# Optimization experiments

Hardware: AMD Instinct MI355X
Metric: run time of the kernel (lower is better)

Reference implementation:

```python
import jax, jax.numpy as jnp
import numpy as np

N = 50000      # nodes
E = 800000     # edges (before self loops)
D = 128        # node feat dim (in = hidden = out)
R_IN = 64      # edge feat in
R_OUT = 64     # edge feat out


def setup_inputs() -> dict:
    key = jax.random.key(0)
    ks = jax.random.split(key, 10)
    src = jax.random.randint(ks[0], (E,), 0, N, dtype=jnp.int32)
    dst = jax.random.randint(ks[1], (E,), 0, N, dtype=jnp.int32)
    x = jax.random.normal(ks[2], (N, D), jnp.float32)
    text_h = jax.random.normal(ks[3], (E, R_IN), jnp.float32)
    s = 1.0 / np.sqrt(D)
    W1 = jax.random.normal(ks[4], (D, D), jnp.float32) * s
    b1 = jnp.zeros((D,), jnp.float32)
    W2 = jax.random.normal(ks[5], (D, D), jnp.float32) * s
    b2 = jnp.zeros((D,), jnp.float32)
    sr = 1.0 / np.sqrt(R_IN)
    relW = jax.random.normal(ks[6], (R_IN, R_OUT), jnp.float32) * sr
    relb = jnp.zeros((R_OUT,), jnp.float32)
    return {"src": src, "dst": dst, "x": x, "text_h": text_h,
            "W1": W1, "b1": b1, "W2": W2, "b2": b2,
            "relW": relW, "relb": relb}


def _graph_conv(h, src, dst, norm_src, norm_dst, W, b, n):
    # DGL GraphConv, norm='both': scale src, gather, segment-sum to dst, scale dst, linear, relu
    h = h * norm_src                                   # [N, D]
    agg = jax.ops.segment_sum(h[src], dst, num_segments=n)  # [N, D]
    h = agg * norm_dst
    return jax.nn.relu(h @ W + b)


def reference(src, dst, x, text_h, W1, b1, W2, b2, relW, relb):
    n = x.shape[0]
    loop = jnp.arange(n, dtype=src.dtype)
    src_a = jnp.concatenate([src, loop])               # add_self_loop
    dst_a = jnp.concatenate([dst, loop])
    ones = jnp.ones(src_a.shape[0], x.dtype)
    out_deg = jax.ops.segment_sum(ones, src_a, num_segments=n)
    in_deg = jax.ops.segment_sum(ones, dst_a, num_segments=n)
    norm_src = (out_deg ** -0.5)[:, None]              # >=1 thanks to self loops
    norm_dst = (in_deg ** -0.5)[:, None]
    h = _graph_conv(x, src_a, dst_a, norm_src, norm_dst, W1, b1, n)
    h = _graph_conv(h, src_a, dst_a, norm_src, norm_dst, W2, b2, n)
    # apply_edges: rel_linear on text_h (self-loop edges get zero-filled text_h)
    text_all = jnp.concatenate([text_h, jnp.zeros((n, text_h.shape[1]), text_h.dtype)])
    e_h = text_all @ relW + relb                       # [E+N, R_OUT]
    # apply_nodes: activation applied once more
    h = jax.nn.relu(h)
    return h, e_h
```

## Files before the change

### kernel.cpp

```cpp
#include <hip/hip_runtime.h>

constexpr int D = 128;
constexpr int R = 64;
constexpr int CAP = 64;
constexpr int OVF_CAP = 65536;
constexpr int TPAD = 68;

typedef float floatx4 __attribute__((ext_vector_type(4)));

static __device__ __forceinline__ float4 f4fma(float a, float4 w, float4 c) {
  c.x = fmaf(a, w.x, c.x); c.y = fmaf(a, w.y, c.y);
  c.z = fmaf(a, w.z, c.z); c.w = fmaf(a, w.w, c.w);
  return c;
}

static __device__ __forceinline__ void nt_store4(float4 v, float* p) {
  floatx4 q; q.x = v.x; q.y = v.y; q.z = v.z; q.w = v.w;
  __builtin_nontemporal_store(q, (floatx4*)p);
}

__global__ void k_init(int* deg_out, int* cursor, int* ovf_cnt, int n) {
  int i = blockIdx.x * blockDim.x + threadIdx.x;
  if (i < n) { deg_out[i] = 1; cursor[i] = 0; }
  if (i == 0) ovf_cnt[0] = 0;
}

__global__ void k_fill(const int* __restrict__ src, const int* __restrict__ dst,
                       int* deg_out, int* cursor, int* bucket,
                       int* ovf_cnt, int2* ovf, int e) {
  int i = blockIdx.x * blockDim.x + threadIdx.x;
  if (i >= e) return;
  int d = dst[i], s = src[i];
  atomicAdd(&deg_out[s], 1);
  int slot = atomicAdd(&cursor[d], 1);
  if (slot < CAP) bucket[(size_t)d * CAP + slot] = s;
  else {
    int oi = atomicAdd(ovf_cnt, 1);
    if (oi < OVF_CAP) ovf[oi] = make_int2(s, d);
  }
}

__global__ void k_norm(const int* __restrict__ deg_out, const int* __restrict__ cursor,
                       float* ns, float* nd, int n) {
  int i = blockIdx.x * blockDim.x + threadIdx.x;
  if (i < n) {
    ns[i] = rsqrtf((float)deg_out[i]);
    nd[i] = rsqrtf((float)(cursor[i] + 1));
  }
}

__global__ __launch_bounds__(256) void k_agg(const float* __restrict__ X,
                                             const float* __restrict__ ns,
                                             const int* __restrict__ cursor,
                                             const int* __restrict__ bucket,
                                             float* __restrict__ agg, int n) {
  int g = threadIdx.x >> 5, lane = threadIdx.x & 31;
  int v = blockIdx.x * 8 + g;
  if (v >= n) return;
  float4 acc;
  {
    float4 xv = ((const float4*)(X + (size_t)v * D))[lane];
    float s = ns[v];
    acc.x = xv.x * s; acc.y = xv.y * s; acc.z = xv.z * s; acc.w = xv.w * s;
  }
  int cnt = min(cursor[v], CAP);
  const int* bk = bucket + (size_t)v * CAP;
  int i = 0;
  for (; i + 4 <= cnt; i += 4) {
    int s0 = bk[i], s1 = bk[i + 1], s2 = bk[i + 2], s3 = bk[i + 3];
    float n0 = ns[s0], n1 = ns[s1], n2 = ns[s2], n3 = ns[s3];
    float4 x0 = ((const float4*)(X + (size_t)s0 * D))[lane];
    float4 x1 = ((const float4*)(X + (size_t)s1 * D))[lane];
    float4 x2 = ((const float4*)(X + (size_t)s2 * D))[lane];
    float4 x3 = ((const float4*)(X + (size_t)s3 * D))[lane];
    acc = f4fma(n0, x0, acc); acc = f4fma(n1, x1, acc);
    acc = f4fma(n2, x2, acc); acc = f4fma(n3, x3, acc);
  }
  for (; i < cnt; ++i) {
    int s0 = bk[i];
    float4 x0 = ((const float4*)(X + (size_t)s0 * D))[lane];
    acc = f4fma(ns[s0], x0, acc);
  }
  ((float4*)(agg + (size_t)v * D))[lane] = acc;
}

__global__ __launch_bounds__(128) void k_ovf(const float* __restrict__ X,
                                             const float* __restrict__ ns,
                                             const int* __restrict__ ovf_cnt,
                                             const int2* __restrict__ ovf,
                                             float* agg) {
  int m = min(ovf_cnt[0], OVF_CAP);
  int t = threadIdx.x;
  for (int i = blockIdx.x; i < m; i += gridDim.x) {
    int2 e = ovf[i];
    atomicAdd(&agg[(size_t)e.y * D + t], X[(size_t)e.x * D + t] * ns[e.x]);
  }
}

__global__ __launch_bounds__(256) void k_gemm_relu(const float* __restrict__ A,
                                                   const float* __restrict__ ndv,
                                                   const float* __restrict__ W,
                                                   const float* __restrict__ bias,
                                                   float* __restrict__ out, int n) {
  __shared__ float Wl[D * D];
  int t = threadIdx.x;
  for (int i = t; i < (D * D) / 4; i += 256) ((float4*)Wl)[i] = ((const float4*)W)[i];
  __syncthreads();

  int ct = t & 15, rg = t >> 4;
  int c0 = ct << 2;
  int row0 = blockIdx.x * 64;

  float4 bb0 = *(const float4*)(bias + c0);
  float4 bb1 = *(const float4*)(bias + c0 + 64);

  int r[4]; const float4* Ap[4];
#pragma unroll
  for (int m = 0; m < 4; ++m) {
    r[m] = row0 + rg + 16 * m;
    int rc = (r[m] < n) ? r[m] : (n - 1);
    Ap[m] = (const float4*)(A + (size_t)rc * D);
  }

  float4 acc[4][2];
#pragma unroll
  for (int m = 0; m < 4; ++m) {
    acc[m][0] = make_float4(0.f, 0.f, 0.f, 0.f);
    acc[m][1] = make_float4(0.f, 0.f, 0.f, 0.f);
  }

#pragma unroll 8
  for (int k4 = 0; k4 < 32; ++k4) {
    float4 a0 = Ap[0][k4], a1 = Ap[1][k4], a2 = Ap[2][k4], a3 = Ap[3][k4];
    const float* wbase = Wl + (k4 << 9) + c0;
#pragma unroll
    for (int kk = 0; kk < 4; ++kk) {
      float4 w0 = *(const float4*)(wbase + (kk << 7));
      float4 w1 = *(const float4*)(wbase + (kk << 7) + 64);
      float e0 = (kk == 0) ? a0.x : (kk == 1) ? a0.y : (kk == 2) ? a0.z : a0.w;
      float e1 = (kk == 0) ? a1.x : (kk == 1) ? a1.y : (kk == 2) ? a1.z : a1.w;
      float e2 = (kk == 0) ? a2.x : (kk == 1) ? a2.y : (kk == 2) ? a2.z : a2.w;
      float e3 = (kk == 0) ? a3.x : (kk == 1) ? a3.y : (kk == 2) ? a3.z : a3.w;
      acc[0][0] = f4fma(e0, w0, acc[0][0]); acc[0][1] = f4fma(e0, w1, acc[0][1]);
      acc[1][0] = f4fma(e1, w0, acc[1][0]); acc[1][1] = f4fma(e1, w1, acc[1][1]);
      acc[2][0] = f4fma(e2, w0, acc[2][0]); acc[2][1] = f4fma(e2, w1, acc[2][1]);
      acc[3][0] = f4fma(e3, w0, acc[3][0]); acc[3][1] = f4fma(e3, w1, acc[3][1]);
    }
  }

#pragma unroll
  for (int m = 0; m < 4; ++m) {
    if (r[m] < n) {
      float ndr = ndv[r[m]];
      float4 o0, o1;
      o0.x = fmaxf(fmaf(acc[m][0].x, ndr, bb0.x), 0.f);
      o0.y = fmaxf(fmaf(acc[m][0].y, ndr, bb0.y), 0.f);
      o0.z = fmaxf(fmaf(acc[m][0].z, ndr, bb0.z), 0.f);
      o0.w = fmaxf(fmaf(acc[m][0].w, ndr, bb0.w), 0.f);
      o1.x = fmaxf(fmaf(acc[m][1].x, ndr, bb1.x), 0.f);
      o1.y = fmaxf(fmaf(acc[m][1].y, ndr, bb1.y), 0.f);
      o1.z = fmaxf(fmaf(acc[m][1].z, ndr, bb1.z), 0.f);
      o1.w = fmaxf(fmaf(acc[m][1].w, ndr, bb1.w), 0.f);
      *(float4*)(out + (size_t)r[m] * D + c0) = o0;
      *(float4*)(out + (size_t)r[m] * D + c0 + 64) = o1;
    }
  }
}

__global__ __launch_bounds__(256) void k_rel(const float* __restrict__ T,
                                             const float* __restrict__ Wr,
                                             const float* __restrict__ br,
                                             float* __restrict__ out,
                                             int e, int ntot) {
  __shared__ float Wl[R * R];
  __shared__ float Tl[64 * TPAD];
  int t = threadIdx.x;
  int tile = blockIdx.x;
  const float4 z4 = make_float4(0.f, 0.f, 0.f, 0.f);

  float4 pre[4];
#pragma unroll
  for (int j = 0; j < 4; ++j) {
    int q = t + 256 * j, rr = q >> 4, c4 = q & 15;
    int grow = tile * 64 + rr;
    pre[j] = (grow < e) ? ((const float4*)T)[(size_t)grow * 16 + c4] : z4;
  }
  for (int i = t; i < (R * R) / 4; i += 256) ((float4*)Wl)[i] = ((const float4*)Wr)[i];
#pragma unroll
  for (int j = 0; j < 4; ++j) {
    int q = t + 256 * j, rr = q >> 4, c4 = q & 15;
    *(float4*)&Tl[rr * TPAD + (c4 << 2)] = pre[j];
  }
  __syncthreads();

  int ct = t & 15, rg = t >> 4;
  int c0 = ct << 2;
  float4 bb = *(const float4*)(br + c0);

  float4 acc0 = bb, acc1 = bb, acc2 = bb, acc3 = bb;
#pragma unroll 4
  for (int k4 = 0; k4 < 16; ++k4) {
    float4 a0 = *(const float4*)&Tl[(rg     ) * TPAD + (k4 << 2)];
    float4 a1 = *(const float4*)&Tl[(rg + 16) * TPAD + (k4 << 2)];
    float4 a2 = *(const float4*)&Tl[(rg + 32) * TPAD + (k4 << 2)];
    float4 a3 = *(const float4*)&Tl[(rg + 48) * TPAD + (k4 << 2)];
    const float* wbase = Wl + (k4 << 8) + c0;
#pragma unroll
    for (int kk = 0; kk < 4; ++kk) {
      float4 w = *(const float4*)(wbase + (kk << 6));
      float e0 = (kk == 0) ? a0.x : (kk == 1) ? a0.y : (kk == 2) ? a0.z : a0.w;
      float e1 = (kk == 0) ? a1.x : (kk == 1) ? a1.y : (kk == 2) ? a1.z : a1.w;
      float e2 = (kk == 0) ? a2.x : (kk == 1) ? a2.y : (kk == 2) ? a2.z : a2.w;
      float e3 = (kk == 0) ? a3.x : (kk == 1) ? a3.y : (kk == 2) ? a3.z : a3.w;
      acc0 = f4fma(e0, w, acc0);
      acc1 = f4fma(e1, w, acc1);
      acc2 = f4fma(e2, w, acc2);
      acc3 = f4fma(e3, w, acc3);
    }
  }

  int base = tile * 64;
  if (base + rg      < ntot) nt_store4(acc0, out + (size_t)(base + rg     ) * R + c0);
  if (base + rg + 16 < ntot) nt_store4(acc1, out + (size_t)(base + rg + 16) * R + c0);
  if (base + rg + 32 < ntot) nt_store4(acc2, out + (size_t)(base + rg + 32) * R + c0);
  if (base + rg + 48 < ntot) nt_store4(acc3, out + (size_t)(base + rg + 48) * R + c0);
}

extern "C" void kernel_launch(void* const* d_in, const int* in_sizes, int n_in,
                              void* d_out, int out_size, void* d_ws, size_t ws_size,
                              hipStream_t stream) {
  const int*   src  = (const int*)d_in[0];
  const int*   dst  = (const int*)d_in[1];
  const float* x    = (const float*)d_in[2];
  const float* text = (const float*)d_in[3];
  const float* W1   = (const float*)d_in[4];
  const float* b1   = (const float*)d_in[5];
  const float* W2   = (const float*)d_in[6];
  const float* b2   = (const float*)d_in[7];
  const float* relW = (const float*)d_in[8];
  const float* relb = (const float*)d_in[9];

  const int E = in_sizes[0];
  const int N = in_sizes[2] / D;

  float* outH = (float*)d_out;
  float* outE = outH + (size_t)N * D;

  char* w = (char*)d_ws;
  auto alloc = [&](size_t bytes) -> void* {
    void* p = (void*)w;
    w += (bytes + 255) & ~(size_t)255;
    return p;
  };
  int*   deg_out  = (int*)alloc((size_t)N * 4);
  int*   cursor   = (int*)alloc((size_t)N * 4);
  float* norm_src = (float*)alloc((size_t)N * 4);
  float* norm_dst = (float*)alloc((size_t)N * 4);
  int*   ovf_cnt  = (int*)alloc(256);
  int2*  ovf      = (int2*)alloc((size_t)OVF_CAP * 8);
  int*   bucket   = (int*)alloc((size_t)N * CAP * 4);
  float* agg      = (float*)alloc((size_t)N * D * 4);

  int nbN = (N + 255) / 256;
  int nbE = (E + 255) / 256;

  k_init<<<nbN, 256, 0, stream>>>(deg_out, cursor, ovf_cnt, N);
  k_fill<<<nbE, 256, 0, stream>>>(src, dst, deg_out, cursor, bucket, ovf_cnt, ovf, E);
  k_norm<<<nbN, 256, 0, stream>>>(deg_out, cursor, norm_src, norm_dst, N);

  k_agg<<<(N + 7) / 8, 256, 0, stream>>>(x, norm_src, cursor, bucket, agg, N);
  k_ovf<<<64, 128, 0, stream>>>(x, norm_src, ovf_cnt, ovf, agg);
  k_gemm_relu<<<(N + 63) / 64, 256, 0, stream>>>(agg, norm_dst, W1, b1, outH, N);

  k_agg<<<(N + 7) / 8, 256, 0, stream>>>(outH, norm_src, cursor, bucket, agg, N);
  k_ovf<<<64, 128, 0, stream>>>(outH, norm_src, ovf_cnt, ovf, agg);
  k_gemm_relu<<<(N + 63) / 64, 256, 0, stream>>>(agg, norm_dst, W2, b2, outH, N);

  int ntot = E + N;
  int nTiles = (ntot + 63) / 64;
  k_rel<<<nTiles, 256, 0, stream>>>(text, relW, relb, outE, E, ntot);
}
```

Measured before the change: 412.6 us.

## Gather pre-scaled bf16 node features in aggregation, fuse source norm into GEMM epilogue

Node features are pre-scaled by the source norm and stored as packed bf16 before each aggregation, either by a new prep kernel for the input or by the first GEMM's epilogue for the hidden layer. The gather kernels then read half as many bytes per neighbor and drop the per-edge norm loads. This targets the memory-bound random gather, at the cost of bf16 rounding error in the aggregated sums and an extra prep pass over x.

```diff
diff --git a/kernel.cpp b/kernel.cpp
--- a/kernel.cpp
+++ b/kernel.cpp
@@ -18,6 +18,19 @@
   floatx4 q; q.x = v.x; q.y = v.y; q.z = v.z; q.w = v.w;
   __builtin_nontemporal_store(q, (floatx4*)p);
 }
+
+static __device__ __forceinline__ float selk(float4 a, int kk) {
+  return (kk == 0) ? a.x : (kk == 1) ? a.y : (kk == 2) ? a.z : a.w;
+}
+
+static __device__ __forceinline__ unsigned pack_bf16x2(float lo, float hi) {
+  unsigned ulo = __float_as_uint(lo), uhi = __float_as_uint(hi);
+  ulo += 0x7FFFu + ((ulo >> 16) & 1u);
+  uhi += 0x7FFFu + ((uhi >> 16) & 1u);
+  return (ulo >> 16) | (uhi & 0xFFFF0000u);
+}
+static __device__ __forceinline__ float bf_lo(unsigned u) { return __uint_as_float(u << 16); }
+static __device__ __forceinline__ float bf_hi(unsigned u) { return __uint_as_float(u & 0xFFFF0000u); }
 
 __global__ void k_init(int* deg_out, int* cursor, int* ovf_cnt, int n) {
   int i = blockIdx.x * blockDim.x + threadIdx.x;
@@ -49,51 +62,69 @@
   }
 }
 
-__global__ __launch_bounds__(256) void k_agg(const float* __restrict__ X,
-                                             const float* __restrict__ ns,
-                                             const int* __restrict__ cursor,
-                                             const int* __restrict__ bucket,
-                                             float* __restrict__ agg, int n) {
+__global__ __launch_bounds__(256) void k_prep(const float* __restrict__ X,
+                                              const float* __restrict__ ns,
+                                              uint4* __restrict__ xs, int n16) {
+  int idx = blockIdx.x * 256 + threadIdx.x;
+  if (idx >= n16) return;
+  int row = idx >> 4, g = idx & 15;
+  const float4* xp = (const float4*)(X + (size_t)row * D + g * 8);
+  float4 a = xp[0], b = xp[1];
+  float s = ns[row];
+  uint4 o;
+  o.x = pack_bf16x2(a.x * s, a.y * s);
+  o.y = pack_bf16x2(a.z * s, a.w * s);
+  o.z = pack_bf16x2(b.x * s, b.y * s);
+  o.w = pack_bf16x2(b.z * s, b.w * s);
+  xs[(size_t)row * 16 + g] = o;
+}
+
+__global__ __launch_bounds__(256) void k_agg_b(const unsigned* __restrict__ XS,
+                                               const int* __restrict__ cursor,
+                                               const int* __restrict__ bucket,
+                                               float* __restrict__ agg, int n) {
   int g = threadIdx.x >> 5, lane = threadIdx.x & 31;
   int v = blockIdx.x * 8 + g;
   if (v >= n) return;
   float4 acc;
   {
-    float4 xv = ((const float4*)(X + (size_t)v * D))[lane];
-    float s = ns[v];
-    acc.x = xv.x * s; acc.y = xv.y * s; acc.z = xv.z * s; acc.w = xv.w * s;
+    uint2 u = ((const uint2*)(XS + (size_t)v * 64))[lane];
+    acc.x = bf_lo(u.x); acc.y = bf_hi(u.x); acc.z = bf_lo(u.y); acc.w = bf_hi(u.y);
   }
   int cnt = min(cursor[v], CAP);
   const int* bk = bucket + (size_t)v * CAP;
   int i = 0;
   for (; i + 4 <= cnt; i += 4) {
     int s0 = bk[i], s1 = bk[i + 1], s2 = bk[i + 2], s3 = bk[i + 3];
-    float n0 = ns[s0], n1 = ns[s1], n2 = ns[s2], n3 = ns[s3];
-    float4 x0 = ((const float4*)(X + (size_t)s0 * D))[lane];
-    float4 x1 = ((const float4*)(X + (size_t)s1 * D))[lane];
-    float4 x2 = ((const float4*)(X + (size_t)s2 * D))[lane];
-    float4 x3 = ((const float4*)(X + (size_t)s3 * D))[lane];
-    acc = f4fma(n0, x0, acc); acc = f4fma(n1, x1, acc);
-    acc = f4fma(n2, x2, acc); acc = f4fma(n3, x3, acc);
+    uint2 u0 = ((const uint2*)(XS + (size_t)s0 * 64))[lane];
+    uint2 u1 = ((const uint2*)(XS + (size_t)s1 * 64))[lane];
+    uint2 u2 = ((const uint2*)(XS + (size_t)s2 * 64))[lane];
+    uint2 u3 = ((const uint2*)(XS + (size_t)s3 * 64))[lane];
+    acc.x += bf_lo(u0.x) + bf_lo(u1.x) + bf_lo(u2.x) + bf_lo(u3.x);
+    acc.y += bf_hi(u0.x) + bf_hi(u1.x) + bf_hi(u2.x) + bf_hi(u3.x);
+    acc.z += bf_lo(u0.y) + bf_lo(u1.y) + bf_lo(u2.y) + bf_lo(u3.y);
+    acc.w += bf_hi(u0.y) + bf_hi(u1.y) + bf_hi(u2.y) + bf_hi(u3.y);
   }
   for (; i < cnt; ++i) {
     int s0 = bk[i];
-    float4 x0 = ((const float4*)(X + (size_t)s0 * D))[lane];
-    acc = f4fma(ns[s0], x0, acc);
+    uint2 u0 = ((const uint2*)(XS + (size_t)s0 * 64))[lane];
+    acc.x += bf_lo(u0.x); acc.y += bf_hi(u0.x);
+    acc.z += bf_lo(u0.y); acc.w += bf_hi(u0.y);
   }
   ((float4*)(agg + (size_t)v * D))[lane] = acc;
 }
 
-__global__ __launch_bounds__(128) void k_ovf(const float* __restrict__ X,
-                                             const float* __restrict__ ns,
-                                             const int* __restrict__ ovf_cnt,
-                                             const int2* __restrict__ ovf,
-                                             float* agg) {
+__global__ __launch_bounds__(128) void k_ovf_b(const unsigned* __restrict__ XS,
+                                               const int* __restrict__ ovf_cnt,
+                                               const int2* __restrict__ ovf,
+                                               float* agg) {
   int m = min(ovf_cnt[0], OVF_CAP);
   int t = threadIdx.x;
   for (int i = blockIdx.x; i < m; i += gridDim.x) {
     int2 e = ovf[i];
-    atomicAdd(&agg[(size_t)e.y * D + t], X[(size_t)e.x * D + t] * ns[e.x]);
+    unsigned u = XS[(size_t)e.x * 64 + (t >> 1)];
+    float f = (t & 1) ? bf_hi(u) : bf_lo(u);
+    atomicAdd(&agg[(size_t)e.y * D + t], f);
   }
 }
 
@@ -101,7 +132,10 @@
                                                    const float* __restrict__ ndv,
                                                    const float* __restrict__ W,
                                                    const float* __restrict__ bias,
-                                                   float* __restrict__ out, int n) {
+                                                   const float* __restrict__ post,
+                                                   float* __restrict__ outf,
+                                                   unsigned* __restrict__ outb,
+                                                   int n) {
   __shared__ float Wl[D * D];
   int t = threadIdx.x;
   for (int i = t; i < (D * D) / 4; i += 256) ((float4*)Wl)[i] = ((const float4*)W)[i];
@@ -137,10 +171,7 @@
     for (int kk = 0; kk < 4; ++kk) {
       float4 w0 = *(const float4*)(wbase + (kk << 7));
       float4 w1 = *(const float4*)(wbase + (kk << 7) + 64);
-      float e0 = (kk == 0) ? a0.x : (kk == 1) ? a0.y : (kk == 2) ? a0.z : a0.w;
-      float e1 = (kk == 0) ? a1.x : (kk == 1) ? a1.y : (kk == 2) ? a1.z : a1.w;
-      float e2 = (kk == 0) ? a2.x : (kk == 1) ? a2.y : (kk == 2) ? a2.z : a2.w;
-      float e3 = (kk == 0) ? a3.x : (kk == 1) ? a3.y : (kk == 2) ? a3.z : a3.w;
+      float e0 = selk(a0, kk), e1 = selk(a1, kk), e2 = selk(a2, kk), e3 = selk(a3, kk);
       acc[0][0] = f4fma(e0, w0, acc[0][0]); acc[0][1] = f4fma(e0, w1, acc[0][1]);
       acc[1][0] = f4fma(e1, w0, acc[1][0]); acc[1][1] = f4fma(e1, w1, acc[1][1]);
       acc[2][0] = f4fma(e2, w0, acc[2][0]); acc[2][1] = f4fma(e2, w1, acc[2][1]);
@@ -161,8 +192,19 @@
       o1.y = fmaxf(fmaf(acc[m][1].y, ndr, bb1.y), 0.f);
       o1.z = fmaxf(fmaf(acc[m][1].z, ndr, bb1.z), 0.f);
       o1.w = fmaxf(fmaf(acc[m][1].w, ndr, bb1.w), 0.f);
-      *(float4*)(out + (size_t)r[m] * D + c0) = o0;
-      *(float4*)(out + (size_t)r[m] * D + c0 + 64) = o1;
+      if (outb) {
+        float ps = post[r[m]];
+        uint2 p0, p1;
+        p0.x = pack_bf16x2(o0.x * ps, o0.y * ps);
+        p0.y = pack_bf16x2(o0.z * ps, o0.w * ps);
+        p1.x = pack_bf16x2(o1.x * ps, o1.y * ps);
+        p1.y = pack_bf16x2(o1.z * ps, o1.w * ps);
+        *(uint2*)(outb + (size_t)r[m] * 64 + (c0 >> 1)) = p0;
+        *(uint2*)(outb + (size_t)r[m] * 64 + (c0 >> 1) + 32) = p1;
+      } else {
+        *(float4*)(outf + (size_t)r[m] * D + c0) = o0;
+        *(float4*)(outf + (size_t)r[m] * D + c0 + 64) = o1;
+      }
     }
   }
 }
@@ -208,10 +250,7 @@
 #pragma unroll
     for (int kk = 0; kk < 4; ++kk) {
       float4 w = *(const float4*)(wbase + (kk << 6));
-      float e0 = (kk == 0) ? a0.x : (kk == 1) ? a0.y : (kk == 2) ? a0.z : a0.w;
-      float e1 = (kk == 0) ? a1.x : (kk == 1) ? a1.y : (kk == 2) ? a1.z : a1.w;
-      float e2 = (kk == 0) ? a2.x : (kk == 1) ? a2.y : (kk == 2) ? a2.z : a2.w;
-      float e3 = (kk == 0) ? a3.x : (kk == 1) ? a3.y : (kk == 2) ? a3.z : a3.w;
+      float e0 = selk(a0, kk), e1 = selk(a1, kk), e2 = selk(a2, kk), e3 = selk(a3, kk);
       acc0 = f4fma(e0, w, acc0);
       acc1 = f4fma(e1, w, acc1);
       acc2 = f4fma(e2, w, acc2);
@@ -252,14 +291,16 @@
     w += (bytes + 255) & ~(size_t)255;
     return p;
   };
-  int*   deg_out  = (int*)alloc((size_t)N * 4);
-  int*   cursor   = (int*)alloc((size_t)N * 4);
-  float* norm_src = (float*)alloc((size_t)N * 4);
-  float* norm_dst = (float*)alloc((size_t)N * 4);
-  int*   ovf_cnt  = (int*)alloc(256);
-  int2*  ovf      = (int2*)alloc((size_t)OVF_CAP * 8);
-  int*   bucket   = (int*)alloc((size_t)N * CAP * 4);
-  float* agg      = (float*)alloc((size_t)N * D * 4);
+  int*      deg_out  = (int*)alloc((size_t)N * 4);
+  int*      cursor   = (int*)alloc((size_t)N * 4);
+  float*    norm_src = (float*)alloc((size_t)N * 4);
+  float*    norm_dst = (float*)alloc((size_t)N * 4);
+  int*      ovf_cnt  = (int*)alloc(256);
+  int2*     ovf      = (int2*)alloc((size_t)OVF_CAP * 8);
+  int*      bucket   = (int*)alloc((size_t)N * CAP * 4);
+  float*    agg      = (float*)alloc((size_t)N * D * 4);
+  unsigned* xs       = (unsigned*)alloc((size_t)N * 64 * 4);
+  unsigned* h1p      = (unsigned*)alloc((size_t)N * 64 * 4);
 
   int nbN = (N + 255) / 256;
   int nbE = (E + 255) / 256;
@@ -268,13 +309,16 @@
   k_fill<<<nbE, 256, 0, stream>>>(src, dst, deg_out, cursor, bucket, ovf_cnt, ovf, E);
   k_norm<<<nbN, 256, 0, stream>>>(deg_out, cursor, norm_src, norm_dst, N);
 
-  k_agg<<<(N + 7) / 8, 256, 0, stream>>>(x, norm_src, cursor, bucket, agg, N);
-  k_ovf<<<64, 128, 0, stream>>>(x, norm_src, ovf_cnt, ovf, agg);
-  k_gemm_relu<<<(N + 63) / 64, 256, 0, stream>>>(agg, norm_dst, W1, b1, outH, N);
-
-  k_agg<<<(N + 7) / 8, 256, 0, stream>>>(outH, norm_src, cursor, bucket, agg, N);
-  k_ovf<<<64, 128, 0, stream>>>(outH, norm_src, ovf_cnt, ovf, agg);
-  k_gemm_relu<<<(N + 63) / 64, 256, 0, stream>>>(agg, norm_dst, W2, b2, outH, N);
+  k_prep<<<(N * 16 + 255) / 256, 256, 0, stream>>>(x, norm_src, (uint4*)xs, N * 16);
+  k_agg_b<<<(N + 7) / 8, 256, 0, stream>>>(xs, cursor, bucket, agg, N);
+  k_ovf_b<<<64, 128, 0, stream>>>(xs, ovf_cnt, ovf, agg);
+  k_gemm_relu<<<(N + 63) / 64, 256, 0, stream>>>(agg, norm_dst, W1, b1, norm_src,
+                                                 nullptr, h1p, N);
+
+  k_agg_b<<<(N + 7) / 8, 256, 0, stream>>>(h1p, cursor, bucket, agg, N);
+  k_ovf_b<<<64, 128, 0, stream>>>(h1p, ovf_cnt, ovf, agg);
+  k_gemm_relu<<<(N + 63) / 64, 256, 0, stream>>>(agg, norm_dst, W2, b2, nullptr,
+                                                 outH, nullptr, N);
 
   int ntot = E + N;
   int nTiles = (ntot + 63) / 64;
```

Measured after the change: 372.4 us. 9.7% less time.
